# Kernel optimization log

Hardware: AMD Instinct MI355X
Metric: run time of the kernel (lower is better)

The kernel has to match this reference:

```python
import jax, jax.numpy as jnp
import numpy as np

B, TQ, TK = 4, 256, 256
Q, K, H = 256, 256, 256


def setup_inputs() -> dict:
    key = jax.random.key(0)
    ks = jax.random.split(key, 10)
    s = 0.05
    return {
        "queries": jax.random.normal(ks[0], (B, TQ, Q), dtype=jnp.float32),
        "keys": jax.random.normal(ks[1], (B, TK, K), dtype=jnp.float32),
        # lengths in [T//2, T] so no fully-masked query rows (torch would NaN there too)
        "query_lengths": jax.random.randint(ks[2], (B,), TQ // 2, TQ + 1),
        "key_lengths": jax.random.randint(ks[3], (B,), TK // 2, TK + 1),
        # nn.Linear(Q+K, H): weight applied as x @ W1; torch concat order is [keys, queries]
        "W1": jax.random.normal(ks[4], (K + Q, H), dtype=jnp.float32) * s,
        "b1": jax.random.normal(ks[5], (H,), dtype=jnp.float32) * s,
        "W2": jax.random.normal(ks[6], (H, H), dtype=jnp.float32) * s,
        "b2": jax.random.normal(ks[7], (H,), dtype=jnp.float32) * s,
        "W3": jax.random.normal(ks[8], (H, 1), dtype=jnp.float32) * s,
        "b3": jax.random.normal(ks[9], (1,), dtype=jnp.float32) * s,
    }


def reference(queries, keys, query_lengths, key_lengths, W1, b1, W2, b2, W3, b3):
    Bn, Tq, Qd = queries.shape
    Tk, Kd = keys.shape[1], keys.shape[2]
    # Split the first linear: concat([keys, queries]) @ W1 == keys@W1[:K] + queries@W1[K:]
    kh = jnp.einsum("bkd,dh->bkh", keys, W1[:Kd])      # [B,Tk,H]
    qh = jnp.einsum("bqd,dh->bqh", queries, W1[Kd:])   # [B,Tq,H]
    h = jax.nn.relu(qh[:, :, None, :] + kh[:, None, :, :] + b1)  # [B,Tq,Tk,H]
    h = jax.nn.relu(jnp.einsum("bqkh,hg->bqkg", h, W2) + b2)     # [B,Tq,Tk,H]
    scores = jnp.einsum("bqkh,h->bqk", h, W3[:, 0]) + b3[0]       # [B,Tq,Tk]
    # mask True where position is padding (query OR key out of range)
    mask = (jnp.arange(Tq)[None, :, None] >= query_lengths[:, None, None]) | (
        jnp.arange(Tk)[None, None, :] >= key_lengths[:, None, None]
    )
    scores = jnp.where(mask, -1e30, scores)
    probs = jax.nn.softmax(scores, axis=-1)
    probs = jnp.where(mask, 0.0, probs)
    return jnp.einsum("bqk,bkd->bqd", probs, keys)  # [B,Tq,K]
```

## Files before the change

### kernel.cpp

```cpp
#include <hip/hip_runtime.h>
#include <cstdint>

#define BATCH 4
#define TQ 256
#define TK 256
#define DIM 256
#define HD 256

typedef _Float16 f16x8 __attribute__((ext_vector_type(8)));
typedef float f32x4 __attribute__((ext_vector_type(4)));

union U4H8 { uint4 u; f16x8 v; };

#define KEEP(x) asm volatile("" : "+v"(x))

__device__ __forceinline__ unsigned short f2h(float f) {
    _Float16 h = (_Float16)f;
    unsigned short u;
    __builtin_memcpy(&u, &h, 2);
    return u;
}

__device__ __forceinline__ f16x8 relu8(f16x8 h) {
    f16x8 z = {};
#if __has_builtin(__builtin_elementwise_max)
    return __builtin_elementwise_max(h, z);
#else
#pragma unroll
    for (int i = 0; i < 8; ++i) h[i] = h[i] > (_Float16)0 ? h[i] : (_Float16)0;
    return h;
#endif
}

__global__ __launch_bounds__(256) void prep_all(
    const float* __restrict__ queries, const float* __restrict__ keys,
    const float* __restrict__ W1, const float* __restrict__ b1,
    const float* __restrict__ W2,
    unsigned short* __restrict__ qhh, unsigned short* __restrict__ khh,
    unsigned short* __restrict__ W2T) {
    int i = blockIdx.x;
    int t = threadIdx.x;
    if (i >= 512) {
        __shared__ float tile[32][33];
        int bi = i - 512;
        int tx = t & 31, ty = t >> 5;
        int tc = (bi & 7) * 32, tn = (bi >> 3) * 32;
#pragma unroll
        for (int r = 0; r < 4; ++r)
            tile[ty + r * 8][tx] = W2[(tc + ty + r * 8) * HD + tn + tx];
        __syncthreads();
#pragma unroll
        for (int r = 0; r < 4; ++r)
            W2T[(tn + ty + r * 8) * HD + tc + tx] = f2h(tile[tx][ty + r * 8]);
        return;
    }
    bool isQ = i < 256;
    int r0 = (i & 255) * 4;
    const float* X = isQ ? queries : keys;
    const float* W = W1 + (isQ ? DIM * HD : 0);
    unsigned short* O = isQ ? qhh : khh;
    __shared__ float4 xs4[4][DIM / 4];
    xs4[t >> 6][t & 63] =
        *(const float4*)(X + (size_t)(r0 + (t >> 6)) * DIM + (t & 63) * 4);
    __syncthreads();
    float acc[4] = {0.f, 0.f, 0.f, 0.f};
#pragma unroll 4
    for (int d4 = 0; d4 < DIM / 4; ++d4) {
        const float4 x0 = xs4[0][d4];
        const float4 x1 = xs4[1][d4];
        const float4 x2 = xs4[2][d4];
        const float4 x3 = xs4[3][d4];
        const float w0 = W[(d4 * 4 + 0) * HD + t];
        const float w1 = W[(d4 * 4 + 1) * HD + t];
        const float w2 = W[(d4 * 4 + 2) * HD + t];
        const float w3 = W[(d4 * 4 + 3) * HD + t];
        acc[0] = fmaf(x0.x, w0, acc[0]); acc[1] = fmaf(x1.x, w0, acc[1]);
        acc[2] = fmaf(x2.x, w0, acc[2]); acc[3] = fmaf(x3.x, w0, acc[3]);
        acc[0] = fmaf(x0.y, w1, acc[0]); acc[1] = fmaf(x1.y, w1, acc[1]);
        acc[2] = fmaf(x2.y, w1, acc[2]); acc[3] = fmaf(x3.y, w1, acc[3]);
        acc[0] = fmaf(x0.z, w2, acc[0]); acc[1] = fmaf(x1.z, w2, acc[1]);
        acc[2] = fmaf(x2.z, w2, acc[2]); acc[3] = fmaf(x3.z, w2, acc[3]);
        acc[0] = fmaf(x0.w, w3, acc[0]); acc[1] = fmaf(x1.w, w3, acc[1]);
        acc[2] = fmaf(x2.w, w3, acc[2]); acc[3] = fmaf(x3.w, w3, acc[3]);
    }
    float bias = isQ ? b1[t] : 0.f;
#pragma unroll
    for (int r = 0; r < 4; ++r)
        O[(size_t)(r0 + r) * HD + t] = f2h(acc[r] + bias);
}

__global__ __launch_bounds__(256, 2) void mlp_attn(
    const unsigned short* __restrict__ qh, const unsigned short* __restrict__ kh,
    const unsigned short* __restrict__ W2T,
    const float* __restrict__ b2, const float* __restrict__ W3,
    const float* __restrict__ keys,
    const int* __restrict__ qlens, const int* __restrict__ klens,
    float* __restrict__ out) {
    int orig = blockIdx.x;
    int task = ((orig & 7) << 6) | (orig >> 3);
    int b = task & 3;
    int q0 = (task >> 2) << 1;
    int t = threadIdx.x;
    int qlen = qlens[b];
    float* orow = out + (b * TQ + q0) * DIM;
    if (q0 >= qlen) { orow[t] = 0.f; orow[DIM + t] = 0.f; return; }
    bool v1 = (q0 + 1) < qlen;
    int klen = klens[b];
    int nch = (klen + 31) >> 5;

    __shared__ uint4 Afrag[8][4][64];
    __shared__ float sprt[4][2][TK];
    __shared__ float srow[2][TK];
    __shared__ uint4 qbuf4[2][HD / 8];
    __shared__ float red[16];

    int w = t >> 6, lane = t & 63;
    int col = lane & 15, quad = lane >> 4;

    int nb = w << 6;
    uint4 bfr[4][8];
#pragma unroll
    for (int nt = 0; nt < 4; ++nt) {
        int n = nb + (nt << 4) + col;
        const uint4* r = (const uint4*)(W2T + n * HD) + quad;
#pragma unroll
        for (int s = 0; s < 8; ++s) bfr[nt][s] = r[s * 4];
    }
    float b2v[4][4], w3v[4][4];
#pragma unroll
    for (int nt = 0; nt < 4; ++nt)
#pragma unroll
        for (int r = 0; r < 4; ++r) {
            int n = nb + (nt << 4) + (quad << 2) + r;
            b2v[nt][r] = b2[n];
            w3v[nt][r] = W3[n];
        }

    int qsel = w >> 1;
    int rsub = ((w & 1) << 4) | col;
    const unsigned short* kbase = kh + (b * TK + rsub) * HD + (quad << 3);

    if (t < 64)
        qbuf4[t >> 5][t & 31] =
            *(const uint4*)(qh + (size_t)(b * TQ + q0 + (t >> 5)) * HD + (t & 31) * 8);

    {
        const unsigned short* qrowg = qh + (b * TQ + q0 + qsel) * HD + (quad << 3);
        uint4* as = &Afrag[0][w][lane];
#pragma unroll
        for (int s = 0; s < 8; ++s) {
            U4H8 kf, qf, h;
            kf.u = *(const uint4*)(kbase + s * 32);
            qf.u = *(const uint4*)(qrowg + s * 32);
            h.v = relu8(kf.v + qf.v);
            as[s * 256] = h.u;
        }
    }

#pragma unroll
    for (int nt = 0; nt < 4; ++nt)
#pragma unroll
        for (int s = 0; s < 8; ++s) {
            KEEP(bfr[nt][s].x); KEEP(bfr[nt][s].y);
            KEEP(bfr[nt][s].z); KEEP(bfr[nt][s].w);
        }

    __syncthreads();

    auto sloop = [&](int mt, f32x4* acc) {
#pragma unroll
        for (int s = 0; s < 8; ++s) {
            U4H8 au;
            au.u = Afrag[s][mt][lane];
#pragma unroll
            for (int nt = 0; nt < 4; ++nt) {
                U4H8 bu;
                bu.u = bfr[nt][s];
                acc[nt] = __builtin_amdgcn_mfma_f32_16x16x32_f16(
                    bu.v, au.v, acc[nt], 0, 0, 0);
            }
        }
    };
    auto epi = [&](int c, int mt, const f32x4* acc) {
        int hf = mt >> 1, m2 = mt & 1;
        float part = 0.f;
#pragma unroll
        for (int nt = 0; nt < 4; ++nt)
#pragma unroll
            for (int r = 0; r < 4; ++r)
                part = fmaf(fmaxf(acc[nt][r] + b2v[nt][r], 0.f), w3v[nt][r], part);
        part += __shfl_xor(part, 16, 64);
        part += __shfl_xor(part, 32, 64);
        if (quad == 0)
            sprt[w][hf][(c << 5) | (m2 << 4) | col] = part;
    };

    for (int c = 0; c < nch; ++c) {
        bool stg = (c + 1 < nch);
        const unsigned short* krow = kbase + (((c + 1) << 5)) * HD;
        uint4 Kst[8];
        if (stg) {
#pragma unroll
            for (int s = 0; s < 8; ++s) Kst[s] = *(const uint4*)(krow + s * 32);
#pragma unroll
            for (int s = 0; s < 8; ++s) {
                KEEP(Kst[s].x); KEEP(Kst[s].y); KEEP(Kst[s].z); KEEP(Kst[s].w);
            }
        }
        __builtin_amdgcn_sched_barrier(0);

        {   f32x4 acc[4] = {}; sloop(0, acc); epi(c, 0, acc); }
        {   f32x4 acc[4] = {}; sloop(1, acc); epi(c, 1, acc); }
        {   f32x4 acc[4] = {}; sloop(2, acc); epi(c, 2, acc); }
        {   f32x4 acc[4] = {}; sloop(3, acc); epi(c, 3, acc); }

        __syncthreads();
        if (stg) {
            uint4* as = &Afrag[0][w][lane];
#pragma unroll
            for (int s = 0; s < 8; ++s) {
                U4H8 kf, qf, h;
                kf.u = Kst[s];
                qf.u = qbuf4[qsel][s * 4 + quad];
                h.v = relu8(kf.v + qf.v);
                as[s * 256] = h.u;
            }
        }
        __syncthreads();
    }

    float s0 = -3.4e38f, s1 = -3.4e38f;
    if (t < klen) {
        s0 = (sprt[0][0][t] + sprt[1][0][t]) + (sprt[2][0][t] + sprt[3][0][t]);
        s1 = (sprt[0][1][t] + sprt[1][1][t]) + (sprt[2][1][t] + sprt[3][1][t]);
    }
    float m0 = s0, m1 = s1;
#pragma unroll
    for (int off = 1; off < 64; off <<= 1) {
        m0 = fmaxf(m0, __shfl_xor(m0, off, 64));
        m1 = fmaxf(m1, __shfl_xor(m1, off, 64));
    }
    if (lane == 0) { red[w] = m0; red[8 + w] = m1; }
    __syncthreads();
    m0 = fmaxf(fmaxf(red[0], red[1]), fmaxf(red[2], red[3]));
    m1 = fmaxf(fmaxf(red[8], red[9]), fmaxf(red[10], red[11]));
    float e0 = (t < klen) ? __expf(s0 - m0) : 0.f;
    float e1 = (t < klen) ? __expf(s1 - m1) : 0.f;
    float u0 = e0, u1 = e1;
#pragma unroll
    for (int off = 1; off < 64; off <<= 1) {
        u0 += __shfl_xor(u0, off, 64);
        u1 += __shfl_xor(u1, off, 64);
    }
    if (lane == 0) { red[4 + w] = u0; red[12 + w] = u1; }
    __syncthreads();
    float d0 = red[4] + red[5] + red[6] + red[7];
    float d1 = red[12] + red[13] + red[14] + red[15];
    srow[0][t] = e0 / d0;
    srow[1][t] = e1 / d1;
    __syncthreads();

    float a0 = 0.f, a1 = 0.f;
    const float* kp = keys + b * TK * DIM + t;
#pragma unroll 16
    for (int k = 0; k < klen; ++k) {
        float v = kp[k * DIM];
        a0 = fmaf(srow[0][k], v, a0);
        a1 = fmaf(srow[1][k], v, a1);
    }
    orow[t] = a0;
    orow[DIM + t] = v1 ? a1 : 0.f;
}

extern "C" void kernel_launch(void* const* d_in, const int* in_sizes, int n_in,
                              void* d_out, int out_size, void* d_ws, size_t ws_size,
                              hipStream_t stream) {
    (void)in_sizes; (void)n_in; (void)out_size; (void)ws_size;
    const float* queries = (const float*)d_in[0];
    const float* keys    = (const float*)d_in[1];
    const int*   qlens   = (const int*)d_in[2];
    const int*   klens   = (const int*)d_in[3];
    const float* W1      = (const float*)d_in[4];
    const float* b1      = (const float*)d_in[5];
    const float* W2      = (const float*)d_in[6];
    const float* b2      = (const float*)d_in[7];
    const float* W3      = (const float*)d_in[8];
    float* out = (float*)d_out;

    unsigned short* qhh = (unsigned short*)d_ws;
    unsigned short* khh = qhh + BATCH * TQ * HD;
    unsigned short* W2T = khh + BATCH * TK * HD;

    prep_all<<<576, 256, 0, stream>>>(queries, keys, W1, b1, W2, qhh, khh, W2T);
    mlp_attn<<<BATCH * TQ / 2, 256, 0, stream>>>(
        qhh, khh, W2T, b2, W3, keys, qlens, klens, out);
}
```

Baseline: 125.5 us.

## Process four query rows per 512-thread block, halving W2 tile per wave

Each block now handles four query rows with eight waves instead of two rows with four waves. Each wave holds a 32-column slice of W2 in registers instead of 64, and runs eight M-tiles per key chunk. The change aims to amortise each key-chunk load and the W2 register fill over more query rows, and to lower register pressure per wave. In exchange it doubles LDS use, halves the grid to 256 blocks, and makes masked-row early exits coarser.

```diff
diff --git a/kernel.cpp b/kernel.cpp
--- a/kernel.cpp
+++ b/kernel.cpp
@@ -89,7 +89,7 @@
         O[(size_t)(r0 + r) * HD + t] = f2h(acc[r] + bias);
 }
 
-__global__ __launch_bounds__(256, 2) void mlp_attn(
+__global__ __launch_bounds__(512, 2) void mlp_attn(
     const unsigned short* __restrict__ qh, const unsigned short* __restrict__ kh,
     const unsigned short* __restrict__ W2T,
     const float* __restrict__ b2, const float* __restrict__ W3,
@@ -97,55 +97,53 @@
     const int* __restrict__ qlens, const int* __restrict__ klens,
     float* __restrict__ out) {
     int orig = blockIdx.x;
-    int task = ((orig & 7) << 6) | (orig >> 3);
+    int task = ((orig & 7) << 5) | (orig >> 3);
     int b = task & 3;
-    int q0 = (task >> 2) << 1;
+    int q0 = (task >> 2) << 2;
     int t = threadIdx.x;
     int qlen = qlens[b];
-    float* orow = out + (b * TQ + q0) * DIM;
-    if (q0 >= qlen) { orow[t] = 0.f; orow[DIM + t] = 0.f; return; }
-    bool v1 = (q0 + 1) < qlen;
+    float* obase = out + ((size_t)b * TQ + q0) * DIM;
+    if (q0 >= qlen) { obase[t] = 0.f; obase[512 + t] = 0.f; return; }
     int klen = klens[b];
     int nch = (klen + 31) >> 5;
 
-    __shared__ uint4 Afrag[8][4][64];
-    __shared__ float sprt[4][2][TK];
-    __shared__ float srow[2][TK];
-    __shared__ uint4 qbuf4[2][HD / 8];
-    __shared__ float red[16];
+    __shared__ uint4 Afrag[8][8][64];
+    __shared__ float sprt[8][4][TK];
+    __shared__ float srow[4][TK];
+    __shared__ uint4 qbuf4[4][HD / 8];
+    __shared__ float redm[4][4], reds[4][4];
 
     int w = t >> 6, lane = t & 63;
     int col = lane & 15, quad = lane >> 4;
 
-    int nb = w << 6;
-    uint4 bfr[4][8];
-#pragma unroll
-    for (int nt = 0; nt < 4; ++nt) {
-        int n = nb + (nt << 4) + col;
+    uint4 bfr[2][8];
+#pragma unroll
+    for (int nt = 0; nt < 2; ++nt) {
+        int n = (w << 5) + (nt << 4) + col;
         const uint4* r = (const uint4*)(W2T + n * HD) + quad;
 #pragma unroll
         for (int s = 0; s < 8; ++s) bfr[nt][s] = r[s * 4];
     }
-    float b2v[4][4], w3v[4][4];
-#pragma unroll
-    for (int nt = 0; nt < 4; ++nt)
+    float b2v[2][4], w3v[2][4];
+#pragma unroll
+    for (int nt = 0; nt < 2; ++nt)
 #pragma unroll
         for (int r = 0; r < 4; ++r) {
-            int n = nb + (nt << 4) + (quad << 2) + r;
+            int n = (w << 5) + (nt << 4) + (quad << 2) + r;
             b2v[nt][r] = b2[n];
             w3v[nt][r] = W3[n];
         }
 
     int qsel = w >> 1;
     int rsub = ((w & 1) << 4) | col;
-    const unsigned short* kbase = kh + (b * TK + rsub) * HD + (quad << 3);
-
-    if (t < 64)
+    const unsigned short* kbase = kh + ((size_t)b * TK + rsub) * HD + (quad << 3);
+
+    if (t < 128)
         qbuf4[t >> 5][t & 31] =
-            *(const uint4*)(qh + (size_t)(b * TQ + q0 + (t >> 5)) * HD + (t & 31) * 8);
+            *(const uint4*)(qh + ((size_t)b * TQ + q0 + (t >> 5)) * HD + (t & 31) * 8);
 
     {
-        const unsigned short* qrowg = qh + (b * TQ + q0 + qsel) * HD + (quad << 3);
+        const unsigned short* qrowg = qh + ((size_t)b * TQ + q0 + qsel) * HD + (quad << 3);
         uint4* as = &Afrag[0][w][lane];
 #pragma unroll
         for (int s = 0; s < 8; ++s) {
@@ -153,12 +151,12 @@
             kf.u = *(const uint4*)(kbase + s * 32);
             qf.u = *(const uint4*)(qrowg + s * 32);
             h.v = relu8(kf.v + qf.v);
-            as[s * 256] = h.u;
-        }
-    }
-
-#pragma unroll
-    for (int nt = 0; nt < 4; ++nt)
+            as[s * 512] = h.u;
+        }
+    }
+
+#pragma unroll
+    for (int nt = 0; nt < 2; ++nt)
 #pragma unroll
         for (int s = 0; s < 8; ++s) {
             KEEP(bfr[nt][s].x); KEEP(bfr[nt][s].y);
@@ -173,7 +171,7 @@
             U4H8 au;
             au.u = Afrag[s][mt][lane];
 #pragma unroll
-            for (int nt = 0; nt < 4; ++nt) {
+            for (int nt = 0; nt < 2; ++nt) {
                 U4H8 bu;
                 bu.u = bfr[nt][s];
                 acc[nt] = __builtin_amdgcn_mfma_f32_16x16x32_f16(
@@ -182,17 +180,17 @@
         }
     };
     auto epi = [&](int c, int mt, const f32x4* acc) {
-        int hf = mt >> 1, m2 = mt & 1;
+        int q = mt >> 1, k16 = mt & 1;
         float part = 0.f;
 #pragma unroll
-        for (int nt = 0; nt < 4; ++nt)
+        for (int nt = 0; nt < 2; ++nt)
 #pragma unroll
             for (int r = 0; r < 4; ++r)
                 part = fmaf(fmaxf(acc[nt][r] + b2v[nt][r], 0.f), w3v[nt][r], part);
         part += __shfl_xor(part, 16, 64);
         part += __shfl_xor(part, 32, 64);
         if (quad == 0)
-            sprt[w][hf][(c << 5) | (m2 << 4) | col] = part;
+            sprt[w][q][(c << 5) | (k16 << 4) | col] = part;
     };
 
     for (int c = 0; c < nch; ++c) {
@@ -209,10 +207,14 @@
         }
         __builtin_amdgcn_sched_barrier(0);
 
-        {   f32x4 acc[4] = {}; sloop(0, acc); epi(c, 0, acc); }
-        {   f32x4 acc[4] = {}; sloop(1, acc); epi(c, 1, acc); }
-        {   f32x4 acc[4] = {}; sloop(2, acc); epi(c, 2, acc); }
-        {   f32x4 acc[4] = {}; sloop(3, acc); epi(c, 3, acc); }
+        {   f32x4 acc[2] = {}; sloop(0, acc); epi(c, 0, acc); }
+        {   f32x4 acc[2] = {}; sloop(1, acc); epi(c, 1, acc); }
+        {   f32x4 acc[2] = {}; sloop(2, acc); epi(c, 2, acc); }
+        {   f32x4 acc[2] = {}; sloop(3, acc); epi(c, 3, acc); }
+        {   f32x4 acc[2] = {}; sloop(4, acc); epi(c, 4, acc); }
+        {   f32x4 acc[2] = {}; sloop(5, acc); epi(c, 5, acc); }
+        {   f32x4 acc[2] = {}; sloop(6, acc); epi(c, 6, acc); }
+        {   f32x4 acc[2] = {}; sloop(7, acc); epi(c, 7, acc); }
 
         __syncthreads();
         if (stg) {
@@ -223,16 +225,21 @@
                 kf.u = Kst[s];
                 qf.u = qbuf4[qsel][s * 4 + quad];
                 h.v = relu8(kf.v + qf.v);
-                as[s * 256] = h.u;
+                as[s * 512] = h.u;
             }
         }
         __syncthreads();
     }
 
+    int g = t >> 8, kk = t & 255;
     float s0 = -3.4e38f, s1 = -3.4e38f;
-    if (t < klen) {
-        s0 = (sprt[0][0][t] + sprt[1][0][t]) + (sprt[2][0][t] + sprt[3][0][t]);
-        s1 = (sprt[0][1][t] + sprt[1][1][t]) + (sprt[2][1][t] + sprt[3][1][t]);
+    if (kk < klen) {
+        s0 = 0.f; s1 = 0.f;
+#pragma unroll
+        for (int wv = 0; wv < 8; ++wv) {
+            s0 += sprt[wv][g][kk];
+            s1 += sprt[wv][g + 2][kk];
+        }
     }
     float m0 = s0, m1 = s1;
 #pragma unroll
@@ -240,36 +247,38 @@
         m0 = fmaxf(m0, __shfl_xor(m0, off, 64));
         m1 = fmaxf(m1, __shfl_xor(m1, off, 64));
     }
-    if (lane == 0) { red[w] = m0; red[8 + w] = m1; }
-    __syncthreads();
-    m0 = fmaxf(fmaxf(red[0], red[1]), fmaxf(red[2], red[3]));
-    m1 = fmaxf(fmaxf(red[8], red[9]), fmaxf(red[10], red[11]));
-    float e0 = (t < klen) ? __expf(s0 - m0) : 0.f;
-    float e1 = (t < klen) ? __expf(s1 - m1) : 0.f;
+    if (lane == 0) { redm[g][w & 3] = m0; redm[g + 2][w & 3] = m1; }
+    __syncthreads();
+    m0 = fmaxf(fmaxf(redm[g][0], redm[g][1]), fmaxf(redm[g][2], redm[g][3]));
+    m1 = fmaxf(fmaxf(redm[g + 2][0], redm[g + 2][1]),
+               fmaxf(redm[g + 2][2], redm[g + 2][3]));
+    float e0 = (kk < klen) ? __expf(s0 - m0) : 0.f;
+    float e1 = (kk < klen) ? __expf(s1 - m1) : 0.f;
     float u0 = e0, u1 = e1;
 #pragma unroll
     for (int off = 1; off < 64; off <<= 1) {
         u0 += __shfl_xor(u0, off, 64);
         u1 += __shfl_xor(u1, off, 64);
     }
-    if (lane == 0) { red[4 + w] = u0; red[12 + w] = u1; }
-    __syncthreads();
-    float d0 = red[4] + red[5] + red[6] + red[7];
-    float d1 = red[12] + red[13] + red[14] + red[15];
-    srow[0][t] = e0 / d0;
-    srow[1][t] = e1 / d1;
+    __syncthreads();
+    if (lane == 0) { reds[g][w & 3] = u0; reds[g + 2][w & 3] = u1; }
+    __syncthreads();
+    float d0 = (reds[g][0] + reds[g][1]) + (reds[g][2] + reds[g][3]);
+    float d1 = (reds[g + 2][0] + reds[g + 2][1]) + (reds[g + 2][2] + reds[g + 2][3]);
+    srow[g][kk] = e0 / d0;
+    srow[g + 2][kk] = e1 / d1;
     __syncthreads();
 
     float a0 = 0.f, a1 = 0.f;
-    const float* kp = keys + b * TK * DIM + t;
+    const float* kp = keys + (size_t)b * TK * DIM + kk;
 #pragma unroll 16
     for (int k = 0; k < klen; ++k) {
         float v = kp[k * DIM];
-        a0 = fmaf(srow[0][k], v, a0);
-        a1 = fmaf(srow[1][k], v, a1);
-    }
-    orow[t] = a0;
-    orow[DIM + t] = v1 ? a1 : 0.f;
+        a0 = fmaf(srow[g][k], v, a0);
+        a1 = fmaf(srow[g + 2][k], v, a1);
+    }
+    obase[g * DIM + kk] = (q0 + g < qlen) ? a0 : 0.f;
+    obase[(g + 2) * DIM + kk] = (q0 + g + 2 < qlen) ? a1 : 0.f;
 }
 
 extern "C" void kernel_launch(void* const* d_in, const int* in_sizes, int n_in,
@@ -292,6 +301,6 @@
     unsigned short* W2T = khh + BATCH * TK * HD;
 
     prep_all<<<576, 256, 0, stream>>>(queries, keys, W1, b1, W2, qhh, khh, W2T);
-    mlp_attn<<<BATCH * TQ / 2, 256, 0, stream>>>(
+    mlp_attn<<<256, 512, 0, stream>>>(
         qhh, khh, W2T, b2, W3, keys, qlens, klens, out);
 }
```

Measured after the change: 132.0 us. 1.05x slower.

## Fuse prep and attention kernels into persistent kernel with grid barrier

Applied to the files above, without the earlier changes.

Merges the projection/transposition prep kernel and the MLP-attention kernel into one persistent 256-block launch that synchronises through a global atomic barrier, so the second launch and its idle gap go away. Each block now does both the query and key projections for its row slice, transposes one W2 row, then processes two attention tasks. The second task index is rotated within groups of four to balance load across batches. In exchange, the grid falls from 512 to 256 blocks, which halves the parallelism in the attention phase. The spin barrier assumes all 256 blocks are resident at once and adds an extra memset launch.

```diff
diff --git a/kernel.cpp b/kernel.cpp
--- a/kernel.cpp
+++ b/kernel.cpp
@@ -32,90 +32,74 @@
 #endif
 }
 
-__global__ __launch_bounds__(256) void prep_all(
+__global__ __launch_bounds__(256, 2) void fused_all(
     const float* __restrict__ queries, const float* __restrict__ keys,
     const float* __restrict__ W1, const float* __restrict__ b1,
-    const float* __restrict__ W2,
+    const float* __restrict__ W2, const float* __restrict__ b2,
+    const float* __restrict__ W3,
+    const int* __restrict__ qlens, const int* __restrict__ klens,
     unsigned short* __restrict__ qhh, unsigned short* __restrict__ khh,
-    unsigned short* __restrict__ W2T) {
+    unsigned short* __restrict__ W2T, unsigned int* __restrict__ gbar,
+    float* __restrict__ out) {
     int i = blockIdx.x;
     int t = threadIdx.x;
-    if (i >= 512) {
-        __shared__ float tile[32][33];
-        int bi = i - 512;
-        int tx = t & 31, ty = t >> 5;
-        int tc = (bi & 7) * 32, tn = (bi >> 3) * 32;
-#pragma unroll
-        for (int r = 0; r < 4; ++r)
-            tile[ty + r * 8][tx] = W2[(tc + ty + r * 8) * HD + tn + tx];
-        __syncthreads();
-#pragma unroll
-        for (int r = 0; r < 4; ++r)
-            W2T[(tn + ty + r * 8) * HD + tc + tx] = f2h(tile[tx][ty + r * 8]);
-        return;
-    }
-    bool isQ = i < 256;
-    int r0 = (i & 255) * 4;
-    const float* X = isQ ? queries : keys;
-    const float* W = W1 + (isQ ? DIM * HD : 0);
-    unsigned short* O = isQ ? qhh : khh;
+    int w = t >> 6, lane = t & 63;
+    int col = lane & 15, quad = lane >> 4;
+
     __shared__ float4 xs4[4][DIM / 4];
-    xs4[t >> 6][t & 63] =
-        *(const float4*)(X + (size_t)(r0 + (t >> 6)) * DIM + (t & 63) * 4);
-    __syncthreads();
-    float acc[4] = {0.f, 0.f, 0.f, 0.f};
-#pragma unroll 4
-    for (int d4 = 0; d4 < DIM / 4; ++d4) {
-        const float4 x0 = xs4[0][d4];
-        const float4 x1 = xs4[1][d4];
-        const float4 x2 = xs4[2][d4];
-        const float4 x3 = xs4[3][d4];
-        const float w0 = W[(d4 * 4 + 0) * HD + t];
-        const float w1 = W[(d4 * 4 + 1) * HD + t];
-        const float w2 = W[(d4 * 4 + 2) * HD + t];
-        const float w3 = W[(d4 * 4 + 3) * HD + t];
-        acc[0] = fmaf(x0.x, w0, acc[0]); acc[1] = fmaf(x1.x, w0, acc[1]);
-        acc[2] = fmaf(x2.x, w0, acc[2]); acc[3] = fmaf(x3.x, w0, acc[3]);
-        acc[0] = fmaf(x0.y, w1, acc[0]); acc[1] = fmaf(x1.y, w1, acc[1]);
-        acc[2] = fmaf(x2.y, w1, acc[2]); acc[3] = fmaf(x3.y, w1, acc[3]);
-        acc[0] = fmaf(x0.z, w2, acc[0]); acc[1] = fmaf(x1.z, w2, acc[1]);
-        acc[2] = fmaf(x2.z, w2, acc[2]); acc[3] = fmaf(x3.z, w2, acc[3]);
-        acc[0] = fmaf(x0.w, w3, acc[0]); acc[1] = fmaf(x1.w, w3, acc[1]);
-        acc[2] = fmaf(x2.w, w3, acc[2]); acc[3] = fmaf(x3.w, w3, acc[3]);
-    }
-    float bias = isQ ? b1[t] : 0.f;
-#pragma unroll
-    for (int r = 0; r < 4; ++r)
-        O[(size_t)(r0 + r) * HD + t] = f2h(acc[r] + bias);
-}
-
-__global__ __launch_bounds__(256, 2) void mlp_attn(
-    const unsigned short* __restrict__ qh, const unsigned short* __restrict__ kh,
-    const unsigned short* __restrict__ W2T,
-    const float* __restrict__ b2, const float* __restrict__ W3,
-    const float* __restrict__ keys,
-    const int* __restrict__ qlens, const int* __restrict__ klens,
-    float* __restrict__ out) {
-    int orig = blockIdx.x;
-    int task = ((orig & 7) << 6) | (orig >> 3);
-    int b = task & 3;
-    int q0 = (task >> 2) << 1;
-    int t = threadIdx.x;
-    int qlen = qlens[b];
-    float* orow = out + (b * TQ + q0) * DIM;
-    if (q0 >= qlen) { orow[t] = 0.f; orow[DIM + t] = 0.f; return; }
-    bool v1 = (q0 + 1) < qlen;
-    int klen = klens[b];
-    int nch = (klen + 31) >> 5;
-
     __shared__ uint4 Afrag[8][4][64];
     __shared__ float sprt[4][2][TK];
     __shared__ float srow[2][TK];
     __shared__ uint4 qbuf4[2][HD / 8];
     __shared__ float red[16];
 
-    int w = t >> 6, lane = t & 63;
-    int col = lane & 15, quad = lane >> 4;
+    W2T[(size_t)i * HD + t] = f2h(W2[(size_t)t * HD + i]);
+
+#pragma unroll 1
+    for (int pass = 0; pass < 2; ++pass) {
+        bool isQ = (pass == 0);
+        const float* X = isQ ? queries : keys;
+        const float* W = W1 + (isQ ? DIM * HD : 0);
+        unsigned short* O = isQ ? qhh : khh;
+        int r0 = i * 4;
+        xs4[t >> 6][t & 63] =
+            *(const float4*)(X + (size_t)(r0 + (t >> 6)) * DIM + (t & 63) * 4);
+        __syncthreads();
+        float acc[4] = {0.f, 0.f, 0.f, 0.f};
+#pragma unroll 4
+        for (int d4 = 0; d4 < DIM / 4; ++d4) {
+            const float4 x0 = xs4[0][d4];
+            const float4 x1 = xs4[1][d4];
+            const float4 x2 = xs4[2][d4];
+            const float4 x3 = xs4[3][d4];
+            const float w0 = W[(d4 * 4 + 0) * HD + t];
+            const float w1 = W[(d4 * 4 + 1) * HD + t];
+            const float w2 = W[(d4 * 4 + 2) * HD + t];
+            const float w3 = W[(d4 * 4 + 3) * HD + t];
+            acc[0] = fmaf(x0.x, w0, acc[0]); acc[1] = fmaf(x1.x, w0, acc[1]);
+            acc[2] = fmaf(x2.x, w0, acc[2]); acc[3] = fmaf(x3.x, w0, acc[3]);
+            acc[0] = fmaf(x0.y, w1, acc[0]); acc[1] = fmaf(x1.y, w1, acc[1]);
+            acc[2] = fmaf(x2.y, w1, acc[2]); acc[3] = fmaf(x3.y, w1, acc[3]);
+            acc[0] = fmaf(x0.z, w2, acc[0]); acc[1] = fmaf(x1.z, w2, acc[1]);
+            acc[2] = fmaf(x2.z, w2, acc[2]); acc[3] = fmaf(x3.z, w2, acc[3]);
+            acc[0] = fmaf(x0.w, w3, acc[0]); acc[1] = fmaf(x1.w, w3, acc[1]);
+            acc[2] = fmaf(x2.w, w3, acc[2]); acc[3] = fmaf(x3.w, w3, acc[3]);
+        }
+        float bias = isQ ? b1[t] : 0.f;
+#pragma unroll
+        for (int r = 0; r < 4; ++r)
+            O[(size_t)(r0 + r) * HD + t] = f2h(acc[r] + bias);
+        __syncthreads();
+    }
+
+    if (t == 0) {
+        __threadfence();
+        atomicAdd(gbar, 1u);
+        while (atomicAdd(gbar, 0u) < 256u)
+            __builtin_amdgcn_s_sleep(8);
+    }
+    __syncthreads();
+    __threadfence();
 
     int nb = w << 6;
     uint4 bfr[4][8];
@@ -135,28 +119,6 @@
             b2v[nt][r] = b2[n];
             w3v[nt][r] = W3[n];
         }
-
-    int qsel = w >> 1;
-    int rsub = ((w & 1) << 4) | col;
-    const unsigned short* kbase = kh + (b * TK + rsub) * HD + (quad << 3);
-
-    if (t < 64)
-        qbuf4[t >> 5][t & 31] =
-            *(const uint4*)(qh + (size_t)(b * TQ + q0 + (t >> 5)) * HD + (t & 31) * 8);
-
-    {
-        const unsigned short* qrowg = qh + (b * TQ + q0 + qsel) * HD + (quad << 3);
-        uint4* as = &Afrag[0][w][lane];
-#pragma unroll
-        for (int s = 0; s < 8; ++s) {
-            U4H8 kf, qf, h;
-            kf.u = *(const uint4*)(kbase + s * 32);
-            qf.u = *(const uint4*)(qrowg + s * 32);
-            h.v = relu8(kf.v + qf.v);
-            as[s * 256] = h.u;
-        }
-    }
-
 #pragma unroll
     for (int nt = 0; nt < 4; ++nt)
 #pragma unroll
@@ -165,111 +127,149 @@
             KEEP(bfr[nt][s].z); KEEP(bfr[nt][s].w);
         }
 
-    __syncthreads();
-
-    auto sloop = [&](int mt, f32x4* acc) {
-#pragma unroll
-        for (int s = 0; s < 8; ++s) {
-            U4H8 au;
-            au.u = Afrag[s][mt][lane];
-#pragma unroll
-            for (int nt = 0; nt < 4; ++nt) {
-                U4H8 bu;
-                bu.u = bfr[nt][s];
-                acc[nt] = __builtin_amdgcn_mfma_f32_16x16x32_f16(
-                    bu.v, au.v, acc[nt], 0, 0, 0);
-            }
-        }
-    };
-    auto epi = [&](int c, int mt, const f32x4* acc) {
-        int hf = mt >> 1, m2 = mt & 1;
-        float part = 0.f;
-#pragma unroll
-        for (int nt = 0; nt < 4; ++nt)
-#pragma unroll
-            for (int r = 0; r < 4; ++r)
-                part = fmaf(fmaxf(acc[nt][r] + b2v[nt][r], 0.f), w3v[nt][r], part);
-        part += __shfl_xor(part, 16, 64);
-        part += __shfl_xor(part, 32, 64);
-        if (quad == 0)
-            sprt[w][hf][(c << 5) | (m2 << 4) | col] = part;
-    };
-
-    for (int c = 0; c < nch; ++c) {
-        bool stg = (c + 1 < nch);
-        const unsigned short* krow = kbase + (((c + 1) << 5)) * HD;
-        uint4 Kst[8];
-        if (stg) {
-#pragma unroll
-            for (int s = 0; s < 8; ++s) Kst[s] = *(const uint4*)(krow + s * 32);
-#pragma unroll
-            for (int s = 0; s < 8; ++s) {
-                KEEP(Kst[s].x); KEEP(Kst[s].y); KEEP(Kst[s].z); KEEP(Kst[s].w);
-            }
-        }
-        __builtin_amdgcn_sched_barrier(0);
-
-        {   f32x4 acc[4] = {}; sloop(0, acc); epi(c, 0, acc); }
-        {   f32x4 acc[4] = {}; sloop(1, acc); epi(c, 1, acc); }
-        {   f32x4 acc[4] = {}; sloop(2, acc); epi(c, 2, acc); }
-        {   f32x4 acc[4] = {}; sloop(3, acc); epi(c, 3, acc); }
-
+    int qsel = w >> 1;
+    int rsub = ((w & 1) << 4) | col;
+
+#pragma unroll 1
+    for (int g = 0; g < 2; ++g) {
+        int task = (g == 0) ? i : (256 + (i & ~3) + ((i + 1) & 3));
+        int b = task & 3;
+        int q0 = (task >> 2) << 1;
+        int qlen = qlens[b];
+        float* orow = out + ((size_t)b * TQ + q0) * DIM;
+        if (q0 >= qlen) {
+            orow[t] = 0.f; orow[DIM + t] = 0.f;
+        } else {
+            bool v1 = (q0 + 1) < qlen;
+            int klen = klens[b];
+            int nch = (klen + 31) >> 5;
+            const unsigned short* kbase =
+                khh + ((size_t)b * TK + rsub) * HD + (quad << 3);
+
+            if (t < 64)
+                qbuf4[t >> 5][t & 31] = *(const uint4*)(
+                    qhh + (size_t)(b * TQ + q0 + (t >> 5)) * HD + (t & 31) * 8);
+
+            {
+                const unsigned short* qrowg =
+                    qhh + (size_t)(b * TQ + q0 + qsel) * HD + (quad << 3);
+                uint4* as = &Afrag[0][w][lane];
+#pragma unroll
+                for (int s = 0; s < 8; ++s) {
+                    U4H8 kf, qf, h;
+                    kf.u = *(const uint4*)(kbase + s * 32);
+                    qf.u = *(const uint4*)(qrowg + s * 32);
+                    h.v = relu8(kf.v + qf.v);
+                    as[s * 256] = h.u;
+                }
+            }
+            __syncthreads();
+
+            for (int c = 0; c < nch; ++c) {
+                bool stg = (c + 1 < nch);
+                const unsigned short* krow = kbase + (((c + 1) << 5)) * HD;
+                uint4 Kst[8];
+                if (stg) {
+#pragma unroll
+                    for (int s = 0; s < 8; ++s)
+                        Kst[s] = *(const uint4*)(krow + s * 32);
+#pragma unroll
+                    for (int s = 0; s < 8; ++s) {
+                        KEEP(Kst[s].x); KEEP(Kst[s].y);
+                        KEEP(Kst[s].z); KEEP(Kst[s].w);
+                    }
+                }
+                __builtin_amdgcn_sched_barrier(0);
+
+#pragma unroll
+                for (int mt = 0; mt < 4; ++mt) {
+                    f32x4 acc[4] = {};
+#pragma unroll
+                    for (int s = 0; s < 8; ++s) {
+                        U4H8 au;
+                        au.u = Afrag[s][mt][lane];
+#pragma unroll
+                        for (int nt = 0; nt < 4; ++nt) {
+                            U4H8 bu;
+                            bu.u = bfr[nt][s];
+                            acc[nt] = __builtin_amdgcn_mfma_f32_16x16x32_f16(
+                                bu.v, au.v, acc[nt], 0, 0, 0);
+                        }
+                    }
+                    float part = 0.f;
+#pragma unroll
+                    for (int nt = 0; nt < 4; ++nt)
+#pragma unroll
+                        for (int r = 0; r < 4; ++r)
+                            part = fmaf(fmaxf(acc[nt][r] + b2v[nt][r], 0.f),
+                                        w3v[nt][r], part);
+                    part += __shfl_xor(part, 16, 64);
+                    part += __shfl_xor(part, 32, 64);
+                    if (quad == 0)
+                        sprt[w][mt >> 1][(c << 5) | ((mt & 1) << 4) | col] = part;
+                }
+
+                __syncthreads();
+                if (stg) {
+                    uint4* as = &Afrag[0][w][lane];
+#pragma unroll
+                    for (int s = 0; s < 8; ++s) {
+                        U4H8 kf, qf, h;
+                        kf.u = Kst[s];
+                        qf.u = qbuf4[qsel][s * 4 + quad];
+                        h.v = relu8(kf.v + qf.v);
+                        as[s * 256] = h.u;
+                    }
+                }
+                __syncthreads();
+            }
+
+            float s0 = -3.4e38f, s1 = -3.4e38f;
+            if (t < klen) {
+                s0 = (sprt[0][0][t] + sprt[1][0][t]) +
+                     (sprt[2][0][t] + sprt[3][0][t]);
+                s1 = (sprt[0][1][t] + sprt[1][1][t]) +
+                     (sprt[2][1][t] + sprt[3][1][t]);
+            }
+            float m0 = s0, m1 = s1;
+#pragma unroll
+            for (int off = 1; off < 64; off <<= 1) {
+                m0 = fmaxf(m0, __shfl_xor(m0, off, 64));
+                m1 = fmaxf(m1, __shfl_xor(m1, off, 64));
+            }
+            if (lane == 0) { red[w] = m0; red[8 + w] = m1; }
+            __syncthreads();
+            m0 = fmaxf(fmaxf(red[0], red[1]), fmaxf(red[2], red[3]));
+            m1 = fmaxf(fmaxf(red[8], red[9]), fmaxf(red[10], red[11]));
+            float e0 = (t < klen) ? __expf(s0 - m0) : 0.f;
+            float e1 = (t < klen) ? __expf(s1 - m1) : 0.f;
+            float u0 = e0, u1 = e1;
+#pragma unroll
+            for (int off = 1; off < 64; off <<= 1) {
+                u0 += __shfl_xor(u0, off, 64);
+                u1 += __shfl_xor(u1, off, 64);
+            }
+            if (lane == 0) { red[4 + w] = u0; red[12 + w] = u1; }
+            __syncthreads();
+            float d0 = red[4] + red[5] + red[6] + red[7];
+            float d1 = red[12] + red[13] + red[14] + red[15];
+            srow[0][t] = e0 / d0;
+            srow[1][t] = e1 / d1;
+            __syncthreads();
+
+            float a0 = 0.f, a1 = 0.f;
+            const float* kp = keys + (size_t)b * TK * DIM + t;
+#pragma unroll 16
+            for (int k = 0; k < klen; ++k) {
+                float v = kp[k * DIM];
+                a0 = fmaf(srow[0][k], v, a0);
+                a1 = fmaf(srow[1][k], v, a1);
+            }
+            orow[t] = a0;
+            orow[DIM + t] = v1 ? a1 : 0.f;
+        }
         __syncthreads();
-        if (stg) {
-            uint4* as = &Afrag[0][w][lane];
-#pragma unroll
-            for (int s = 0; s < 8; ++s) {
-                U4H8 kf, qf, h;
-                kf.u = Kst[s];
-                qf.u = qbuf4[qsel][s * 4 + quad];
-                h.v = relu8(kf.v + qf.v);
-                as[s * 256] = h.u;
-            }
-        }
-        __syncthreads();
-    }
-
-    float s0 = -3.4e38f, s1 = -3.4e38f;
-    if (t < klen) {
-        s0 = (sprt[0][0][t] + sprt[1][0][t]) + (sprt[2][0][t] + sprt[3][0][t]);
-        s1 = (sprt[0][1][t] + sprt[1][1][t]) + (sprt[2][1][t] + sprt[3][1][t]);
-    }
-    float m0 = s0, m1 = s1;
-#pragma unroll
-    for (int off = 1; off < 64; off <<= 1) {
-        m0 = fmaxf(m0, __shfl_xor(m0, off, 64));
-        m1 = fmaxf(m1, __shfl_xor(m1, off, 64));
-    }
-    if (lane == 0) { red[w] = m0; red[8 + w] = m1; }
-    __syncthreads();
-    m0 = fmaxf(fmaxf(red[0], red[1]), fmaxf(red[2], red[3]));
-    m1 = fmaxf(fmaxf(red[8], red[9]), fmaxf(red[10], red[11]));
-    float e0 = (t < klen) ? __expf(s0 - m0) : 0.f;
-    float e1 = (t < klen) ? __expf(s1 - m1) : 0.f;
-    float u0 = e0, u1 = e1;
-#pragma unroll
-    for (int off = 1; off < 64; off <<= 1) {
-        u0 += __shfl_xor(u0, off, 64);
-        u1 += __shfl_xor(u1, off, 64);
-    }
-    if (lane == 0) { red[4 + w] = u0; red[12 + w] = u1; }
-    __syncthreads();
-    float d0 = red[4] + red[5] + red[6] + red[7];
-    float d1 = red[12] + red[13] + red[14] + red[15];
-    srow[0][t] = e0 / d0;
-    srow[1][t] = e1 / d1;
-    __syncthreads();
-
-    float a0 = 0.f, a1 = 0.f;
-    const float* kp = keys + b * TK * DIM + t;
-#pragma unroll 16
-    for (int k = 0; k < klen; ++k) {
-        float v = kp[k * DIM];
-        a0 = fmaf(srow[0][k], v, a0);
-        a1 = fmaf(srow[1][k], v, a1);
-    }
-    orow[t] = a0;
-    orow[DIM + t] = v1 ? a1 : 0.f;
+    }
 }
 
 extern "C" void kernel_launch(void* const* d_in, const int* in_sizes, int n_in,
@@ -290,8 +290,10 @@
     unsigned short* qhh = (unsigned short*)d_ws;
     unsigned short* khh = qhh + BATCH * TQ * HD;
     unsigned short* W2T = khh + BATCH * TK * HD;
-
-    prep_all<<<576, 256, 0, stream>>>(queries, keys, W1, b1, W2, qhh, khh, W2T);
-    mlp_attn<<<BATCH * TQ / 2, 256, 0, stream>>>(
-        qhh, khh, W2T, b2, W3, keys, qlens, klens, out);
-}
+    unsigned int* gbar = (unsigned int*)(W2T + HD * HD);
+
+    hipMemsetAsync(gbar, 0, sizeof(unsigned int), stream);
+    fused_all<<<256, 256, 0, stream>>>(
+        queries, keys, W1, b1, W2, b2, W3, qlens, klens,
+        qhh, khh, W2T, gbar, out);
+}
```

New measurement: 256.6 us. 2.04x slower.
